# Performance work log

Hardware: AMD Instinct MI355X
Metric: run time of the kernel (lower is better)

## Reference

```python
import jax, jax.numpy as jnp
import numpy as np

B, L = 2, 4096
EMBED_DIM, NUM_HEADS, WINDOW = 1024, 16, 256
NUM_EXPERTS, TOP_K, FF_HIDDEN = 8, 2, 4096
ENTROPY_W, MAX_USAGE = 0.1, 0.3


def setup_inputs() -> dict:
    key = jax.random.key(0)
    ks = jax.random.split(key, 10)
    s = 0.02
    C, F, E = EMBED_DIM, FF_HIDDEN, NUM_EXPERTS
    return {
        "x": jax.random.normal(ks[0], (B, L, C), jnp.float32),
        "g1": jnp.ones((C,), jnp.float32), "b1": jnp.zeros((C,), jnp.float32),
        "g2": jnp.ones((C,), jnp.float32), "b2": jnp.zeros((C,), jnp.float32),
        "g3": jnp.ones((C,), jnp.float32), "b3": jnp.zeros((C,), jnp.float32),
        "Wqkv": jax.random.normal(ks[1], (C, 3 * C), jnp.float32) * s, "bqkv": jnp.zeros((3 * C,), jnp.float32),
        "Wo": jax.random.normal(ks[2], (C, C), jnp.float32) * s, "bo": jnp.zeros((C,), jnp.float32),
        "conv_w": jax.random.normal(ks[3], (C, C, 3), jnp.float32) * s, "conv_b": jnp.zeros((C,), jnp.float32),
        "gate_W": jax.random.normal(ks[4], (C, E), jnp.float32) * s, "gate_b": jnp.zeros((E,), jnp.float32),
        "expert_W": jax.random.normal(ks[5], (E, C, C), jnp.float32) * s, "expert_b": jnp.zeros((E, C), jnp.float32),
        "ff_W1": jax.random.normal(ks[6], (C, F), jnp.float32) * s, "ff_b1": jnp.zeros((F,), jnp.float32),
        "ff_W2": jax.random.normal(ks[7], (F, C), jnp.float32) * s, "ff_b2": jnp.zeros((C,), jnp.float32),
    }


def _ln(x, g, b):
    mu = x.mean(-1, keepdims=True)
    var = ((x - mu) ** 2).mean(-1, keepdims=True)
    return (x - mu) * jax.lax.rsqrt(var + 1e-5) * g + b


def _local_attn(x, Wqkv, bqkv, Wo, bo):
    # Faithful port of the unfold-based overlapping-window attention
    Bsz, Ln, C = x.shape
    hd = C // NUM_HEADS
    pad = (-Ln) % WINDOW
    xp = jnp.pad(x, ((0, 0), (0, pad), (0, 0)))
    Lp = Ln + pad
    qkv = (xp @ Wqkv + bqkv).reshape(Bsz, Lp, 3, NUM_HEADS, hd).transpose(2, 0, 3, 1, 4)
    q, k, v = qkv[0], qkv[1], qkv[2]  # [B,H,Lp,hd]
    step = WINDOW // 2  # bidirectional=True -> overlapping windows
    nw = (Lp - WINDOW) // step + 1
    idx = (jnp.arange(nw) * step)[:, None] + jnp.arange(WINDOW)[None, :]  # [nw,w]

    def win(t):
        # torch unfold(dim=2,size=w,step) puts window on LAST axis -> [B,H,nw,hd,w]
        return jnp.swapaxes(t[:, :, idx, :], -1, -2)

    qw, kw, vw = win(q), win(k), win(v)
    # q @ k^T over the window axis (exactly what the torch code computes)
    attn = jax.nn.softmax(jnp.einsum('bhnds,bhnes->bhnde', qw, kw) * hd ** -0.5, axis=-1)
    o = jnp.einsum('bhnde,bhnes->bhnds', attn, vw)  # [B,H,nw,hd,w]
    o = o.reshape(Bsz, NUM_HEADS, nw * WINDOW, hd).transpose(0, 2, 1, 3).reshape(Bsz, nw * WINDOW, C)
    return (o @ Wo + bo)[:, :Ln]


def _dconv(x, w, b):
    # Conv1d(C,C,k=3,dilation=2,padding='same'); w is [O,I,K]
    y = jax.lax.conv_general_dilated(jnp.swapaxes(x, 1, 2), w, (1,), 'SAME',
                                     rhs_dilation=(2,), dimension_numbers=('NCH', 'OIH', 'NCH'))
    return jnp.swapaxes(y + b[None, :, None], 1, 2)


def _moe(x, gW, gb, eW, eb):
    Bsz, S, C = x.shape
    N = Bsz * S
    xf = x.reshape(N, C)
    probs = jax.nn.softmax(xf @ gW + gb, axis=-1)
    entropy = -jnp.sum(probs * jnp.log(probs + 1e-10), axis=-1).mean()
    topk_p, topk_i = jax.lax.top_k(probs, TOP_K)  # [N,K]
    # dense-equivalent top-k dispatch: out[n] = sum_k p_k * expert_{i_k}(x_n)
    eo = jnp.einsum('nc,ech->neh', xf, eW) + eb  # [N,E,C]
    combine = jnp.zeros((N, NUM_EXPERTS), xf.dtype).at[jnp.arange(N)[:, None], topk_i].add(topk_p)
    out = jnp.einsum('neh,ne->nh', eo, combine)
    counts = jnp.zeros((NUM_EXPERTS,), jnp.float32).at[topk_i.reshape(-1)].add(1.0)
    penalty = jnp.sum(jax.nn.relu(counts / N - MAX_USAGE))
    return out.reshape(Bsz, S, C), ENTROPY_W * entropy + penalty


def reference(x, g1, b1, g2, b2, g3, b3, Wqkv, bqkv, Wo, bo, conv_w, conv_b,
              gate_W, gate_b, expert_W, expert_b, ff_W1, ff_b1, ff_W2, ff_b2):
    x = x + _local_attn(_ln(x, g1, b1), Wqkv, bqkv, Wo, bo)
    x = x + _dconv(_ln(x, g2, b2), conv_w, conv_b)
    moe_out, aux = _moe(_ln(x, g3, b3), gate_W, gate_b, expert_W, expert_b)
    x = x + moe_out
    x = x + (jax.nn.gelu(x @ ff_W1 + ff_b1, approximate=False) @ ff_W2 + ff_b2)
    return x, aux
```

## Files before the change

### kernel.cpp

```cpp
#include <hip/hip_runtime.h>
#include <cmath>

typedef _Float16 f16;
typedef __attribute__((ext_vector_type(8))) _Float16 f16x8;
typedef __attribute__((ext_vector_type(4))) _Float16 f16x4;
typedef __attribute__((ext_vector_type(4))) float f32x4;

struct TileInfo { int m0, mcnt, e, pad; };

__device__ __forceinline__ void gload16(const void* g, void* l) {
  __builtin_amdgcn_global_load_lds((const __attribute__((address_space(1))) void*)g,
                                   (__attribute__((address_space(3))) void*)l, 16, 0, 0);
}

__device__ __forceinline__ float fast_gelu(float u) {
  const float c = u * (0.7978845608028654f + 0.0356774081f * u * u);
  const float t = fminf(2.0f * c, 80.0f);
  const float e = __expf(t);
  return u * (e * __builtin_amdgcn_rcpf(e + 1.0f));
}

template<int NPASS, int MODE, int EPI>
__global__ __launch_bounds__(256)
void gemm_kernel(const f16* __restrict__ Ah, const f16* __restrict__ Al, int lda,
                 const f16* __restrict__ Bh, const f16* __restrict__ Bl, int ldb,
                 const float* __restrict__ bias, const float* __restrict__ res,
                 float* __restrict__ outf, f16* __restrict__ outh, int ldo, int K,
                 const int* __restrict__ rowmap, const TileInfo* __restrict__ table,
                 const char* __restrict__ zbuf) {
  __shared__ __align__(16) char lds[65536];

  const int tid  = threadIdx.x;
  const int wave = tid >> 6;
  const int lane = tid & 63;

  int m0, mcnt, eidx = 0;
  if (MODE == 2) {
    TileInfo ti = table[blockIdx.x];
    if (ti.mcnt <= 0) return;
    m0 = ti.m0; mcnt = ti.mcnt; eidx = ti.e;
  } else { m0 = blockIdx.x * 128; mcnt = 128; }
  const int n0 = blockIdx.y * 128;

  const f16* Bh_ = Bh;
  const float* bias_ = bias;
  size_t adelta = 0, bdelta = 0;
  if (NPASS == 3) {
    adelta = (size_t)((const char*)Al - (const char*)Ah);
    bdelta = (size_t)((const char*)Bl - (const char*)Bh);
  }
  if (MODE == 2) { Bh_ += ((size_t)eidx << 20); bias_ += eidx * 1024; }

  f32x4 acc[4][4] = {};
  const int wm  = (wave >> 1) * 64;
  const int wn  = (wave & 1) * 64;
  const int fr  = lane & 15;
  const int kgb = (lane >> 4) * 16;
  const int wuni = wave * 1024;

  const int sr    = tid / 8;
  const int cbyte = (tid % 8) * 16;

  if constexpr (NPASS == 1) {
    const char* aSrc[4];
    const char* bSrc[4];
    #pragma unroll
    for (int r = 0; r < 4; ++r) {
      const int mr  = sr + r * 32;
      const int cbs = cbyte ^ ((mr & 7) << 4);
      int gi = m0 + ((mr < mcnt) ? mr : (mcnt - 1));
      if (MODE == 1 || MODE == 2) gi = rowmap[gi];
      aSrc[r] = (const char*)Ah + (size_t)gi * lda * 2 + cbs;
      bSrc[r] = (const char*)Bh_ + (size_t)(n0 + mr) * ldb * 2 + cbs;
    }
    const int NT = K / 64;
    #pragma unroll
    for (int r = 0; r < 4; ++r) {
      gload16(aSrc[r], lds + r * 4096 + wuni);
      gload16(bSrc[r], lds + 16384 + r * 4096 + wuni);
    }
    #pragma unroll
    for (int r = 0; r < 4; ++r) {
      gload16(aSrc[r] + 128, lds + 32768 + r * 4096 + wuni);
      gload16(bSrc[r] + 128, lds + 32768 + 16384 + r * 4096 + wuni);
    }
    asm volatile("s_waitcnt vmcnt(8)" ::: "memory");
    __builtin_amdgcn_s_barrier();

    for (int kt = 0; kt < NT; ++kt) {
      const int c = kt & 1;
      const char* LAp = lds + c * 32768;
      const char* LBp = LAp + 16384;
      f16x8 ah[2][4], bh[2][4];
      #pragma unroll
      for (int kk = 0; kk < 2; ++kk) {
        #pragma unroll
        for (int i = 0; i < 4; ++i) {
          const int ar = wm + i * 16 + fr;
          ah[kk][i] = *(const f16x8*)(LAp + ar * 128 + ((kk * 64 + kgb) ^ ((ar & 7) << 4)));
          const int br = wn + i * 16 + fr;
          bh[kk][i] = *(const f16x8*)(LBp + br * 128 + ((kk * 64 + kgb) ^ ((br & 7) << 4)));
        }
      }
      asm volatile("s_waitcnt lgkmcnt(0)" ::: "memory");
      __builtin_amdgcn_s_barrier();
      if (kt + 2 < NT) {
        const size_t ko = (size_t)(kt + 2) * 128;
        #pragma unroll
        for (int r = 0; r < 4; ++r) {
          gload16(aSrc[r] + ko, lds + c * 32768 + r * 4096 + wuni);
          gload16(bSrc[r] + ko, lds + c * 32768 + 16384 + r * 4096 + wuni);
        }
      }
      #pragma unroll
      for (int kk = 0; kk < 2; ++kk)
        #pragma unroll
        for (int i = 0; i < 4; ++i)
          #pragma unroll
          for (int j = 0; j < 4; ++j)
            acc[i][j] = __builtin_amdgcn_mfma_f32_16x16x32_f16(ah[kk][i], bh[kk][j], acc[i][j], 0, 0, 0);
      if (kt + 2 < NT) asm volatile("s_waitcnt vmcnt(8)" ::: "memory");
      else             asm volatile("s_waitcnt vmcnt(0)" ::: "memory");
      __builtin_amdgcn_s_barrier();
    }
  } else {
    const char* aSrcB[4]; const char* bSrcB[4];
    int aRowC[4], aCbs[4];
    #pragma unroll
    for (int r = 0; r < 4; ++r) {
      const int mr  = sr + r * 32;
      const int cbs = cbyte ^ ((mr & 7) << 4);
      int gi = m0 + mr;
      if (MODE == 1) gi = rowmap[gi];
      if (MODE == 3) { aRowC[r] = gi; aCbs[r] = cbs; aSrcB[r] = nullptr; }
      else           { aSrcB[r] = (const char*)Ah + (size_t)gi * lda * 2 + cbs; aRowC[r] = 0; aCbs[r] = 0; }
      bSrcB[r] = (const char*)Bh_ + (size_t)(n0 + mr) * ldb * 2 + cbs;
    }
    const int NT = K / 64;
    f32x4 st[16];

    auto SLOAD = [&](int k0) {
      #pragma unroll
      for (int r = 0; r < 4; ++r) {
        const char* as; const char* asl;
        if (MODE == 3) {
          const int tap = k0 >> 10;
          const int kc  = k0 & 1023;
          const int tok = aRowC[r] & 4095;
          const int stk = tok + (tap - 1) * 2;
          if (stk >= 0 && stk < 4096) {
            as  = (const char*)Ah + (size_t)(aRowC[r] + (tap - 1) * 2) * 2048 + kc * 2 + aCbs[r];
            asl = as + adelta;
          } else { as = zbuf; asl = zbuf; }
        } else {
          as  = aSrcB[r] + (size_t)k0 * 2;
          asl = as + adelta;
        }
        st[r * 4 + 0] = *(const f32x4*)as;
        st[r * 4 + 1] = *(const f32x4*)asl;
        const char* bs = bSrcB[r] + (size_t)k0 * 2;
        st[r * 4 + 2] = *(const f32x4*)bs;
        st[r * 4 + 3] = *(const f32x4*)(bs + bdelta);
      }
    };
    auto SWRITE = [&]() {
      #pragma unroll
      for (int r = 0; r < 4; ++r) {
        *(f32x4*)(lds + 0     + r * 4096 + tid * 16) = st[r * 4 + 0];
        *(f32x4*)(lds + 16384 + r * 4096 + tid * 16) = st[r * 4 + 1];
        *(f32x4*)(lds + 32768 + r * 4096 + tid * 16) = st[r * 4 + 2];
        *(f32x4*)(lds + 49152 + r * 4096 + tid * 16) = st[r * 4 + 3];
      }
    };

    SLOAD(0);
    SWRITE();
    __syncthreads();

    for (int kt = 0; kt < NT; ++kt) {
      if (kt + 1 < NT) SLOAD((kt + 1) * 64);
      #pragma unroll
      for (int kk = 0; kk < 2; ++kk) {
        f16x8 ah[4], al[4], bh[4], bl[4];
        #pragma unroll
        for (int i = 0; i < 4; ++i) {
          const int ar = wm + i * 16 + fr;
          const int ao = ar * 128 + ((kk * 64 + kgb) ^ ((ar & 7) << 4));
          ah[i] = *(const f16x8*)(lds + ao);
          al[i] = *(const f16x8*)(lds + 16384 + ao);
          const int br = wn + i * 16 + fr;
          const int bo = br * 128 + ((kk * 64 + kgb) ^ ((br & 7) << 4));
          bh[i] = *(const f16x8*)(lds + 32768 + bo);
          bl[i] = *(const f16x8*)(lds + 49152 + bo);
        }
        #pragma unroll
        for (int i = 0; i < 4; ++i) {
          #pragma unroll
          for (int j = 0; j < 4; ++j) {
            acc[i][j] = __builtin_amdgcn_mfma_f32_16x16x32_f16(ah[i], bh[j], acc[i][j], 0, 0, 0);
            acc[i][j] = __builtin_amdgcn_mfma_f32_16x16x32_f16(ah[i], bl[j], acc[i][j], 0, 0, 0);
            acc[i][j] = __builtin_amdgcn_mfma_f32_16x16x32_f16(al[i], bh[j], acc[i][j], 0, 0, 0);
          }
        }
      }
      asm volatile("s_waitcnt lgkmcnt(0)" ::: "memory");
      __builtin_amdgcn_s_barrier();
      if (kt + 1 < NT) {
        SWRITE();
        asm volatile("s_waitcnt lgkmcnt(0)" ::: "memory");
      }
      __builtin_amdgcn_s_barrier();
    }
  }

  #pragma unroll
  for (int i = 0; i < 4; ++i) {
    const int mb = wm + i * 16 + (lane >> 4) * 4;
    #pragma unroll
    for (int j = 0; j < 4; ++j) {
      const int nc = n0 + wn + j * 16 + fr;
      const float bv = bias_[nc];
      #pragma unroll
      for (int q = 0; q < 4; ++q) {
        const int ml = mb + q;
        if (MODE == 2 && ml >= mcnt) continue;
        const size_t orow = (size_t)(m0 + ml);
        float v = acc[i][j][q] + bv;
        if (EPI == 1) v += res[orow * ldo + nc];
        if (EPI == 3) v = fast_gelu(v);
        if (EPI <= 1) outf[orow * ldo + nc] = v;
        else          outh[orow * ldo + nc] = (f16)v;
      }
    }
  }
}

template<int WLO, int WGATE>
__global__ __launch_bounds__(256)
void ln_kernel(const float* __restrict__ x, const float* __restrict__ g, const float* __restrict__ b,
               f16* __restrict__ oh, f16* __restrict__ ol,
               const float* __restrict__ gW, const float* __restrict__ gb,
               float* __restrict__ logits) {
  const int row = blockIdx.x;
  const int t = threadIdx.x;
  const float4 v = ((const float4*)(x + (size_t)row * 1024))[t];
  float s  = v.x + v.y + v.z + v.w;
  float ss = v.x * v.x + v.y * v.y + v.z * v.z + v.w * v.w;
  #pragma unroll
  for (int off = 32; off; off >>= 1) { s += __shfl_down(s, off, 64); ss += __shfl_down(ss, off, 64); }
  __shared__ float red[8];
  if ((t & 63) == 0) { red[t >> 6] = s; red[(t >> 6) + 4] = ss; }
  __syncthreads();
  s  = red[0] + red[1] + red[2] + red[3];
  ss = red[4] + red[5] + red[6] + red[7];
  const float mu  = s * (1.0f / 1024.0f);
  const float var = ss * (1.0f / 1024.0f) - mu * mu;
  const float inv = 1.0f / sqrtf(var + 1e-5f);
  const float4 gv = ((const float4*)g)[t];
  const float4 bv = ((const float4*)b)[t];
  float y[4];
  y[0] = (v.x - mu) * inv * gv.x + bv.x;
  y[1] = (v.y - mu) * inv * gv.y + bv.y;
  y[2] = (v.z - mu) * inv * gv.z + bv.z;
  y[3] = (v.w - mu) * inv * gv.w + bv.w;
  f16x4 hv;
  #pragma unroll
  for (int u = 0; u < 4; ++u) hv[u] = (f16)y[u];
  *(f16x4*)(oh + (size_t)row * 1024 + t * 4) = hv;
  if (WLO) {
    f16x4 lv;
    #pragma unroll
    for (int u = 0; u < 4; ++u) lv[u] = (f16)(y[u] - (float)hv[u]);
    *(f16x4*)(ol + (size_t)row * 1024 + t * 4) = lv;
  }
  if (WGATE) {
    const float* gr = gW + (size_t)(t * 4) * 8;
    float lg[8];
    #pragma unroll
    for (int e = 0; e < 8; ++e)
      lg[e] = y[0] * gr[e] + y[1] * gr[8 + e] + y[2] * gr[16 + e] + y[3] * gr[24 + e];
    #pragma unroll
    for (int m = 1; m < 64; m <<= 1)
      #pragma unroll
      for (int e = 0; e < 8; ++e) lg[e] += __shfl_xor(lg[e], m, 64);
    __shared__ float gred[4][8];
    if ((t & 63) == 0) {
      #pragma unroll
      for (int e = 0; e < 8; ++e) gred[t >> 6][e] = lg[e];
    }
    __syncthreads();
    if (t < 8)
      logits[(size_t)row * 8 + t] = gred[0][t] + gred[1][t] + gred[2][t] + gred[3][t] + gb[t];
  }
}

__global__ __launch_bounds__(512, 4)
void attn_kernel(const float* __restrict__ qkv, f16* __restrict__ oh, f16* __restrict__ ol) {
  __shared__ __align__(16) char sm[81920];
  const int bid = blockIdx.x;
  const int b = bid >> 8, h = (bid >> 4) & 15, n = bid & 15;
  const int t = threadIdx.x;
  const size_t rowbase = (size_t)(b * 2176 + n * 128);
  const char* qg = (const char*)(qkv + rowbase * 3072 + h * 64);
  const char* kg = qg + 4096;
  const char* vg = qg + 8192;

  const int srow = t >> 4;
  const int scol = (t & 15) * 16;
  const int wuni = (t >> 6) * 1024;

  const int dt = t >> 4;
  const int et = t & 15;
  float pacc[2][4] = {};

  for (int r = 0; r < 2; ++r) {
    #pragma unroll
    for (int p = 0; p < 4; ++p) {
      const size_t off = (size_t)(r * 128 + p * 32 + srow) * 12288 + scol;
      gload16(qg + off, sm + p * 8192 + wuni);
      gload16(kg + off, sm + 32768 + p * 8192 + wuni);
    }
    __syncthreads();
    #pragma unroll 4
    for (int s = 0; s < 128; ++s) {
      const float2 q2 = *(const float2*)(sm + s * 256 + dt * 8);
      const f32x4 k4 = *(const f32x4*)(sm + 32768 + s * 256 + et * 16);
      #pragma unroll
      for (int z = 0; z < 4; ++z) {
        pacc[0][z] += q2.x * k4[z];
        pacc[1][z] += q2.y * k4[z];
      }
    }
    __syncthreads();
  }

  #pragma unroll
  for (int i = 0; i < 2; ++i) {
    #pragma unroll
    for (int z = 0; z < 4; ++z) pacc[i][z] *= 0.125f;
    float m = fmaxf(fmaxf(pacc[i][0], pacc[i][1]), fmaxf(pacc[i][2], pacc[i][3]));
    m = fmaxf(m, __shfl_xor(m, 1, 16));
    m = fmaxf(m, __shfl_xor(m, 2, 16));
    m = fmaxf(m, __shfl_xor(m, 4, 16));
    m = fmaxf(m, __shfl_xor(m, 8, 16));
    float den = 0.0f;
    #pragma unroll
    for (int z = 0; z < 4; ++z) { pacc[i][z] = __expf(pacc[i][z] - m); den += pacc[i][z]; }
    den += __shfl_xor(den, 1, 16);
    den += __shfl_xor(den, 2, 16);
    den += __shfl_xor(den, 4, 16);
    den += __shfl_xor(den, 8, 16);
    const float dinv = 1.0f / den;
    f32x4 pv;
    #pragma unroll
    for (int z = 0; z < 4; ++z) pv[z] = pacc[i][z] * dinv;
    *(f32x4*)(sm + 65536 + (dt * 2 + i) * 256 + et * 16) = pv;
  }

  const int dt2 = t & 15;
  const int st  = t >> 4;
  const int ch  = h * 64 + (st & 15) * 4;
  const size_t rb2 = (size_t)(b * 4096 + n * 256);

  for (int c = 0; c < 2; ++c) {
    __syncthreads();
    #pragma unroll
    for (int p = 0; p < 4; ++p) {
      const size_t off = (size_t)(c * 128 + p * 32 + srow) * 12288 + scol;
      gload16(vg + off, sm + p * 8192 + wuni);
    }
    __syncthreads();
    float o[16];
    #pragma unroll
    for (int u = 0; u < 16; ++u) o[u] = 0.0f;
    #pragma unroll 2
    for (int e4 = 0; e4 < 16; ++e4) {
      f32x4 p4[4], v4[4];
      #pragma unroll
      for (int i = 0; i < 4; ++i)
        p4[i] = *(const f32x4*)(sm + 65536 + (dt2 * 4 + i) * 256 + e4 * 16);
      #pragma unroll
      for (int j = 0; j < 4; ++j)
        v4[j] = *(const f32x4*)(sm + (st * 4 + j) * 256 + e4 * 16);
      #pragma unroll
      for (int j = 0; j < 4; ++j)
        #pragma unroll
        for (int i = 0; i < 4; ++i) {
          o[j * 4 + i] += v4[j][0] * p4[i][0] + v4[j][1] * p4[i][1]
                        + v4[j][2] * p4[i][2] + v4[j][3] * p4[i][3];
        }
    }
    const int rq = c * 2 + (st >> 4);
    #pragma unroll
    for (int i = 0; i < 4; ++i) {
      const size_t row = rb2 + (size_t)(dt2 * 4 + i) * 4 + rq;
      f16x4 hv, lv;
      #pragma unroll
      for (int j = 0; j < 4; ++j) {
        const float val = o[j * 4 + i];
        hv[j] = (f16)val;
        lv[j] = (f16)(val - (float)hv[j]);
      }
      *(f16x4*)(oh + row * 1024 + ch) = hv;
      *(f16x4*)(ol + row * 1024 + ch) = lv;
    }
  }
}

template<int SPLIT>
__global__ __launch_bounds__(256)
void transpose_kernel(const float* __restrict__ in, int R, int Cc,
                      f16* __restrict__ oh, f16* __restrict__ ol) {
  __shared__ float tile[32][33];
  const size_t mat = (size_t)blockIdx.z * R * Cc;
  in += mat; oh += mat; if (SPLIT) ol += mat;
  const int tx = threadIdx.x & 31, ty = threadIdx.x >> 5;
  const int c = blockIdx.x * 32 + tx;
  #pragma unroll
  for (int j = 0; j < 32; j += 8) {
    const int r = blockIdx.y * 32 + ty + j;
    tile[ty + j][tx] = in[(size_t)r * Cc + c];
  }
  __syncthreads();
  const int rT = blockIdx.y * 32 + tx;
  #pragma unroll
  for (int j = 0; j < 32; j += 8) {
    const int cT = blockIdx.x * 32 + ty + j;
    const float v = tile[tx][ty + j];
    const f16 hv = (f16)v;
    oh[(size_t)cT * R + rT] = hv;
    if (SPLIT) ol[(size_t)cT * R + rT] = (f16)(v - (float)hv);
  }
}

__global__ __launch_bounds__(256)
void convw_kernel(const float* __restrict__ w, f16* __restrict__ oh, f16* __restrict__ ol) {
  const int id = blockIdx.x * 256 + threadIdx.x;
  const int o = id >> 10, i = id & 1023;
  const float* ws = w + (size_t)o * 3072 + i * 3;
  #pragma unroll
  for (int tap = 0; tap < 3; ++tap) {
    const float v = ws[tap];
    const f16 hv = (f16)v;
    const size_t oi = (size_t)o * 3072 + tap * 1024 + i;
    oh[oi] = hv;
    ol[oi] = (f16)(v - (float)hv);
  }
}

__global__ void qkvrows_kernel(int* __restrict__ rows) {
  const int r = blockIdx.x * 256 + threadIdx.x;
  if (r < 4352) rows[r] = (r >= 2176) ? (4096 + r - 2176) : r;
}

__global__ __launch_bounds__(256)
void gatefin_kernel(const float* __restrict__ logits, float* __restrict__ top2p,
                    int* __restrict__ top2i, float* __restrict__ ent,
                    int* __restrict__ counts) {
  __shared__ int hist[8];
  const int t = threadIdx.x;
  if (t < 8) hist[t] = 0;
  __syncthreads();
  const int token = blockIdx.x * 256 + t;
  float lg[8];
  const float4 l0 = ((const float4*)(logits + (size_t)token * 8))[0];
  const float4 l1 = ((const float4*)(logits + (size_t)token * 8))[1];
  lg[0] = l0.x; lg[1] = l0.y; lg[2] = l0.z; lg[3] = l0.w;
  lg[4] = l1.x; lg[5] = l1.y; lg[6] = l1.z; lg[7] = l1.w;
  int i0 = 0; float v0 = lg[0];
  #pragma unroll
  for (int e = 1; e < 8; ++e) if (lg[e] > v0) { v0 = lg[e]; i0 = e; }
  int i1 = 0; float v1 = -1e30f;
  #pragma unroll
  for (int e = 0; e < 8; ++e) if (e != i0 && lg[e] > v1) { v1 = lg[e]; i1 = e; }
  float den = 0.0f; float pr[8];
  #pragma unroll
  for (int e = 0; e < 8; ++e) { pr[e] = __expf(lg[e] - v0); den += pr[e]; }
  const float dinv = 1.0f / den;
  float H = 0.0f, p0 = 0.0f, p1 = 0.0f;
  #pragma unroll
  for (int e = 0; e < 8; ++e) {
    const float p = pr[e] * dinv;
    H -= p * __logf(p + 1e-10f);
    if (e == i0) p0 = p;
    if (e == i1) p1 = p;
  }
  ent[token] = H;
  top2p[token * 2] = p0; top2p[token * 2 + 1] = p1;
  top2i[token * 2] = i0; top2i[token * 2 + 1] = i1;
  atomicAdd(&hist[i0], 1);
  atomicAdd(&hist[i1], 1);
  __syncthreads();
  if (t < 8) atomicAdd(&counts[t], hist[t]);
}

__global__ __launch_bounds__(256)
void scan_kernel(const float* __restrict__ ent, const int* __restrict__ counts,
                 int* __restrict__ offs, TileInfo* __restrict__ table, float* __restrict__ auxout) {
  __shared__ float red[256];
  const int t = threadIdx.x;
  float s = 0.0f;
  for (int k = 0; k < 32; ++k) s += ent[t + (k << 8)];
  red[t] = s; __syncthreads();
  for (int hh = 128; hh > 0; hh >>= 1) { if (t < hh) red[t] += red[t + hh]; __syncthreads(); }
  if (t == 0) {
    const float entmean = red[0] * (1.0f / 8192.0f);
    float pen = 0.0f; int off = 0; int nt = 0;
    for (int e = 0; e < 8; ++e) {
      const int c = counts[e];
      offs[e] = off;
      for (int m = 0; m < c; m += 128) {
        table[nt].m0 = off + m;
        table[nt].mcnt = (c - m < 128) ? (c - m) : 128;
        table[nt].e = e; table[nt].pad = 0;
        ++nt;
      }
      off += c;
      const float fr = (float)c * (1.0f / 8192.0f) - 0.3f;
      pen += (fr > 0.0f) ? fr : 0.0f;
    }
    for (; nt < 160; ++nt) { table[nt].m0 = 0; table[nt].mcnt = 0; table[nt].e = 0; table[nt].pad = 0; }
    auxout[0] = 0.1f * entmean + pen;
  }
}

__global__ __launch_bounds__(256)
void scatter_kernel(const int* __restrict__ top2i, const int* __restrict__ offs,
                    int* __restrict__ fill, int* __restrict__ moe_rows,
                    int* __restrict__ row2slot) {
  __shared__ int hist[8];
  __shared__ int base[8];
  const int t = threadIdx.x;
  if (t < 8) hist[t] = 0;
  __syncthreads();
  const int id = blockIdx.x * 256 + t;
  const int e = top2i[id];
  const int myrank = atomicAdd(&hist[e], 1);
  __syncthreads();
  if (t < 8) base[t] = atomicAdd(&fill[t], hist[t]);
  __syncthreads();
  const int row = offs[e] + base[e] + myrank;
  moe_rows[row] = id >> 1;
  row2slot[id] = row;
}

__global__ __launch_bounds__(256)
void combine_kernel(const float* __restrict__ x2, const f16* __restrict__ eo,
                    const float* __restrict__ top2p, const int* __restrict__ row2slot,
                    float* __restrict__ x3, f16* __restrict__ x3h) {
  const int n = blockIdx.x;
  const int t = threadIdx.x;
  const int r0 = row2slot[n * 2], r1 = row2slot[n * 2 + 1];
  const float p0 = top2p[n * 2], p1 = top2p[n * 2 + 1];
  const float4 xv = ((const float4*)(x2 + (size_t)n * 1024))[t];
  const f16x4 e0 = ((const f16x4*)(eo + (size_t)r0 * 1024))[t];
  const f16x4 e1 = ((const f16x4*)(eo + (size_t)r1 * 1024))[t];
  float4 o;
  o.x = xv.x + p0 * (float)e0[0] + p1 * (float)e1[0];
  o.y = xv.y + p0 * (float)e0[1] + p1 * (float)e1[1];
  o.z = xv.z + p0 * (float)e0[2] + p1 * (float)e1[2];
  o.w = xv.w + p0 * (float)e0[3] + p1 * (float)e1[3];
  ((float4*)(x3 + (size_t)n * 1024))[t] = o;
  f16x4 hv; hv[0] = (f16)o.x; hv[1] = (f16)o.y; hv[2] = (f16)o.z; hv[3] = (f16)o.w;
  ((f16x4*)(x3h + (size_t)n * 1024))[t] = hv;
}

extern "C" void kernel_launch(void* const* d_in, const int* in_sizes, int n_in,
                              void* d_out, int out_size, void* d_ws, size_t ws_size,
                              hipStream_t stream) {
  (void)in_sizes; (void)n_in; (void)out_size; (void)ws_size;
  const float* x     = (const float*)d_in[0];
  const float* g1    = (const float*)d_in[1];
  const float* b1    = (const float*)d_in[2];
  const float* g2    = (const float*)d_in[3];
  const float* b2    = (const float*)d_in[4];
  const float* g3    = (const float*)d_in[5];
  const float* b3    = (const float*)d_in[6];
  const float* Wqkv  = (const float*)d_in[7];
  const float* bqkv  = (const float*)d_in[8];
  const float* Wo    = (const float*)d_in[9];
  const float* bo    = (const float*)d_in[10];
  const float* convw = (const float*)d_in[11];
  const float* convb = (const float*)d_in[12];
  const float* gateW = (const float*)d_in[13];
  const float* gateb = (const float*)d_in[14];
  const float* expW  = (const float*)d_in[15];
  const float* expb  = (const float*)d_in[16];
  const float* ffW1  = (const float*)d_in[17];
  const float* ffb1  = (const float*)d_in[18];
  const float* ffW2  = (const float*)d_in[19];
  const float* ffb2  = (const float*)d_in[20];
  float* out = (float*)d_out;

  char* W = (char*)d_ws;
  f16* wqkvT_h = (f16*)(W + 0);
  f16* wqkvT_l = (f16*)(W + 6291456);
  f16* woT_h   = (f16*)(W + 12582912);
  f16* woT_l   = (f16*)(W + 14680064);
  f16* wcvT_h  = (f16*)(W + 16777216);
  f16* wcvT_l  = (f16*)(W + 23068672);
  f16* wexpT   = (f16*)(W + 29360128);
  f16* wff1T   = (f16*)(W + 46137344);
  f16* wff2T   = (f16*)(W + 54525952);
  char* META   = W + 62914560;
  int* counts    = (int*)(META);
  int* fill      = (int*)(META + 32);
  int* offs      = (int*)(META + 64);
  TileInfo* table = (TileInfo*)(META + 128);
  char* zbuf     = META + 3072;
  int* qkv_rows  = (int*)(META + 4096);
  float* ent     = (float*)(META + 24576);
  float* top2p   = (float*)(META + 57344);
  int* top2i     = (int*)(META + 122880);
  int* moe_rows  = (int*)(META + 188416);
  int* row2slot  = (int*)(META + 253952);
  float* logits  = (float*)(META + 327680);
  char* SA = W + 63963136;
  char* SB = W + 97517568;
  char* SC = W + 164626432;
  char* SD = W + 198180864;
  char* SE = W + 231735296;

  f16* ln1h = (f16*)SA;            f16* ln1l = (f16*)(SA + 16777216);
  f16* ln2h = ln1h;                f16* ln2l = ln1l;
  f16* ln3h = ln1h;                f16* x3h  = (f16*)(SA + 16777216);
  float* qkvbuf = (float*)SB;
  float* x2buf  = (float*)SB;
  f16*   hbuf   = (f16*)SB;
  f16* attnh = (f16*)SC;           f16* attnl = (f16*)(SC + 16777216);
  float* x1 = (float*)SD;
  f16* eobuf = (f16*)SD;
  float* x3 = (float*)SE;

  hipMemsetAsync((void*)META, 0, 4096, stream);

  dim3 blk(256);
  transpose_kernel<1><<<dim3(96, 32, 1), blk, 0, stream>>>(Wqkv, 1024, 3072, wqkvT_h, wqkvT_l);
  transpose_kernel<1><<<dim3(32, 32, 1), blk, 0, stream>>>(Wo, 1024, 1024, woT_h, woT_l);
  convw_kernel<<<4096, blk, 0, stream>>>(convw, wcvT_h, wcvT_l);
  transpose_kernel<0><<<dim3(32, 32, 8), blk, 0, stream>>>(expW, 1024, 1024, wexpT, nullptr);
  transpose_kernel<0><<<dim3(128, 32, 1), blk, 0, stream>>>(ffW1, 1024, 4096, wff1T, nullptr);
  transpose_kernel<0><<<dim3(32, 128, 1), blk, 0, stream>>>(ffW2, 4096, 1024, wff2T, nullptr);
  qkvrows_kernel<<<17, blk, 0, stream>>>(qkv_rows);

  ln_kernel<1, 0><<<8192, blk, 0, stream>>>(x, g1, b1, ln1h, ln1l, nullptr, nullptr, nullptr);
  gemm_kernel<3, 1, 0><<<dim3(34, 24), blk, 0, stream>>>(ln1h, ln1l, 1024, wqkvT_h, wqkvT_l, 1024,
      bqkv, nullptr, qkvbuf, nullptr, 3072, 1024, qkv_rows, nullptr, nullptr);
  attn_kernel<<<512, dim3(512), 0, stream>>>(qkvbuf, attnh, attnl);
  gemm_kernel<3, 0, 1><<<dim3(64, 8), blk, 0, stream>>>(attnh, attnl, 1024, woT_h, woT_l, 1024,
      bo, x, x1, nullptr, 1024, 1024, nullptr, nullptr, nullptr);
  ln_kernel<1, 0><<<8192, blk, 0, stream>>>(x1, g2, b2, ln2h, ln2l, nullptr, nullptr, nullptr);
  gemm_kernel<3, 3, 1><<<dim3(64, 8), blk, 0, stream>>>(ln2h, ln2l, 1024, wcvT_h, wcvT_l, 3072,
      convb, x1, x2buf, nullptr, 1024, 3072, nullptr, nullptr, zbuf);
  ln_kernel<0, 1><<<8192, blk, 0, stream>>>(x2buf, g3, b3, ln3h, nullptr, gateW, gateb, logits);
  gatefin_kernel<<<32, blk, 0, stream>>>(logits, top2p, top2i, ent, counts);
  scan_kernel<<<1, blk, 0, stream>>>(ent, counts, offs, table, out + 8388608);
  scatter_kernel<<<64, blk, 0, stream>>>(top2i, offs, fill, moe_rows, row2slot);
  gemm_kernel<1, 2, 2><<<dim3(136, 8), blk, 0, stream>>>(ln3h, nullptr, 1024, wexpT, nullptr, 1024,
      expb, nullptr, nullptr, eobuf, 1024, 1024, moe_rows, table, nullptr);
  combine_kernel<<<8192, blk, 0, stream>>>(x2buf, eobuf, top2p, row2slot, x3, x3h);
  gemm_kernel<1, 0, 3><<<dim3(64, 32), blk, 0, stream>>>(x3h, nullptr, 1024, wff1T, nullptr, 1024,
      ffb1, nullptr, nullptr, hbuf, 4096, 1024, nullptr, nullptr, nullptr);
  gemm_kernel<1, 0, 1><<<dim3(64, 8), blk, 0, stream>>>(hbuf, nullptr, 4096, wff2T, nullptr, 4096,
      ffb2, x3, out, nullptr, 1024, 4096, nullptr, nullptr, nullptr);
}
```

Measured before the change: 765.3 us.

## Use direct global-to-LDS loads, swizzle block order, compact LN1 rows

The 3-pass GEMM path now loads tiles straight into LDS with global_load_lds instead of staging them through registers. Because there is only one LDS buffer, each step waits at a barrier before compute, which drops the register prefetch overlap. Block indices are remapped so consecutive launched blocks are spread across eight groups of the tile grid, aiming for better cache locality. LN1 now writes only the rows the QKV GEMM uses, in compacted order, which removes the rowmap kernel and halves LN1 work.

New measurement: 786.5 us. 2.8% more time.

```diff
diff --git a/kernel.cpp b/kernel.cpp
--- a/kernel.cpp
+++ b/kernel.cpp
@@ -34,13 +34,20 @@
   const int wave = tid >> 6;
   const int lane = tid & 63;
 
+  const int gx  = gridDim.x;
+  const int lid = blockIdx.x + blockIdx.y * gx;
+  const int per = (gx * gridDim.y) >> 3;
+  const int swz = (lid & 7) * per + (lid >> 3);
+  const int bx  = swz % gx;
+  const int by  = swz / gx;
+
   int m0, mcnt, eidx = 0;
   if (MODE == 2) {
-    TileInfo ti = table[blockIdx.x];
+    TileInfo ti = table[bx];
     if (ti.mcnt <= 0) return;
     m0 = ti.m0; mcnt = ti.mcnt; eidx = ti.e;
-  } else { m0 = blockIdx.x * 128; mcnt = 128; }
-  const int n0 = blockIdx.y * 128;
+  } else { m0 = bx * 128; mcnt = 128; }
+  const int n0 = by * 128;
 
   const f16* Bh_ = Bh;
   const float* bias_ = bias;
@@ -136,10 +143,7 @@
       else           { aSrcB[r] = (const char*)Ah + (size_t)gi * lda * 2 + cbs; aRowC[r] = 0; aCbs[r] = 0; }
       bSrcB[r] = (const char*)Bh_ + (size_t)(n0 + mr) * ldb * 2 + cbs;
     }
-    const int NT = K / 64;
-    f32x4 st[16];
-
-    auto SLOAD = [&](int k0) {
+    for (int k0 = 0; k0 < K; k0 += 64) {
       #pragma unroll
       for (int r = 0; r < 4; ++r) {
         const char* as; const char* asl;
@@ -156,29 +160,13 @@
           as  = aSrcB[r] + (size_t)k0 * 2;
           asl = as + adelta;
         }
-        st[r * 4 + 0] = *(const f32x4*)as;
-        st[r * 4 + 1] = *(const f32x4*)asl;
+        gload16(as,  lds + 0     + r * 4096 + wuni);
+        gload16(asl, lds + 16384 + r * 4096 + wuni);
         const char* bs = bSrcB[r] + (size_t)k0 * 2;
-        st[r * 4 + 2] = *(const f32x4*)bs;
-        st[r * 4 + 3] = *(const f32x4*)(bs + bdelta);
-      }
-    };
-    auto SWRITE = [&]() {
-      #pragma unroll
-      for (int r = 0; r < 4; ++r) {
-        *(f32x4*)(lds + 0     + r * 4096 + tid * 16) = st[r * 4 + 0];
-        *(f32x4*)(lds + 16384 + r * 4096 + tid * 16) = st[r * 4 + 1];
-        *(f32x4*)(lds + 32768 + r * 4096 + tid * 16) = st[r * 4 + 2];
-        *(f32x4*)(lds + 49152 + r * 4096 + tid * 16) = st[r * 4 + 3];
-      }
-    };
-
-    SLOAD(0);
-    SWRITE();
-    __syncthreads();
-
-    for (int kt = 0; kt < NT; ++kt) {
-      if (kt + 1 < NT) SLOAD((kt + 1) * 64);
+        gload16(bs,          lds + 32768 + r * 4096 + wuni);
+        gload16(bs + bdelta, lds + 49152 + r * 4096 + wuni);
+      }
+      __syncthreads();
       #pragma unroll
       for (int kk = 0; kk < 2; ++kk) {
         f16x8 ah[4], al[4], bh[4], bl[4];
@@ -203,13 +191,7 @@
           }
         }
       }
-      asm volatile("s_waitcnt lgkmcnt(0)" ::: "memory");
-      __builtin_amdgcn_s_barrier();
-      if (kt + 1 < NT) {
-        SWRITE();
-        asm volatile("s_waitcnt lgkmcnt(0)" ::: "memory");
-      }
-      __builtin_amdgcn_s_barrier();
+      __syncthreads();
     }
   }
 
@@ -235,15 +217,16 @@
   }
 }
 
-template<int WLO, int WGATE>
+template<int WLO, int WGATE, int COMPACT>
 __global__ __launch_bounds__(256)
 void ln_kernel(const float* __restrict__ x, const float* __restrict__ g, const float* __restrict__ b,
                f16* __restrict__ oh, f16* __restrict__ ol,
                const float* __restrict__ gW, const float* __restrict__ gb,
                float* __restrict__ logits) {
   const int row = blockIdx.x;
+  const int srow = COMPACT ? ((row < 2176) ? row : row + 1920) : row;
   const int t = threadIdx.x;
-  const float4 v = ((const float4*)(x + (size_t)row * 1024))[t];
+  const float4 v = ((const float4*)(x + (size_t)srow * 1024))[t];
   float s  = v.x + v.y + v.z + v.w;
   float ss = v.x * v.x + v.y * v.y + v.z * v.z + v.w * v.w;
   #pragma unroll
@@ -446,11 +429,6 @@
     oh[oi] = hv;
     ol[oi] = (f16)(v - (float)hv);
   }
-}
-
-__global__ void qkvrows_kernel(int* __restrict__ rows) {
-  const int r = blockIdx.x * 256 + threadIdx.x;
-  if (r < 4352) rows[r] = (r >= 2176) ? (4096 + r - 2176) : r;
 }
 
 __global__ __launch_bounds__(256)
@@ -608,7 +586,6 @@
   int* offs      = (int*)(META + 64);
   TileInfo* table = (TileInfo*)(META + 128);
   char* zbuf     = META + 3072;
-  int* qkv_rows  = (int*)(META + 4096);
   float* ent     = (float*)(META + 24576);
   float* top2p   = (float*)(META + 57344);
   int* top2i     = (int*)(META + 122880);
@@ -641,18 +618,17 @@
   transpose_kernel<0><<<dim3(32, 32, 8), blk, 0, stream>>>(expW, 1024, 1024, wexpT, nullptr);
   transpose_kernel<0><<<dim3(128, 32, 1), blk, 0, stream>>>(ffW1, 1024, 4096, wff1T, nullptr);
   transpose_kernel<0><<<dim3(32, 128, 1), blk, 0, stream>>>(ffW2, 4096, 1024, wff2T, nullptr);
-  qkvrows_kernel<<<17, blk, 0, stream>>>(qkv_rows);
-
-  ln_kernel<1, 0><<<8192, blk, 0, stream>>>(x, g1, b1, ln1h, ln1l, nullptr, nullptr, nullptr);
-  gemm_kernel<3, 1, 0><<<dim3(34, 24), blk, 0, stream>>>(ln1h, ln1l, 1024, wqkvT_h, wqkvT_l, 1024,
-      bqkv, nullptr, qkvbuf, nullptr, 3072, 1024, qkv_rows, nullptr, nullptr);
+
+  ln_kernel<1, 0, 1><<<4352, blk, 0, stream>>>(x, g1, b1, ln1h, ln1l, nullptr, nullptr, nullptr);
+  gemm_kernel<3, 0, 0><<<dim3(34, 24), blk, 0, stream>>>(ln1h, ln1l, 1024, wqkvT_h, wqkvT_l, 1024,
+      bqkv, nullptr, qkvbuf, nullptr, 3072, 1024, nullptr, nullptr, nullptr);
   attn_kernel<<<512, dim3(512), 0, stream>>>(qkvbuf, attnh, attnl);
   gemm_kernel<3, 0, 1><<<dim3(64, 8), blk, 0, stream>>>(attnh, attnl, 1024, woT_h, woT_l, 1024,
       bo, x, x1, nullptr, 1024, 1024, nullptr, nullptr, nullptr);
-  ln_kernel<1, 0><<<8192, blk, 0, stream>>>(x1, g2, b2, ln2h, ln2l, nullptr, nullptr, nullptr);
+  ln_kernel<1, 0, 0><<<8192, blk, 0, stream>>>(x1, g2, b2, ln2h, ln2l, nullptr, nullptr, nullptr);
   gemm_kernel<3, 3, 1><<<dim3(64, 8), blk, 0, stream>>>(ln2h, ln2l, 1024, wcvT_h, wcvT_l, 3072,
       convb, x1, x2buf, nullptr, 1024, 3072, nullptr, nullptr, zbuf);
-  ln_kernel<0, 1><<<8192, blk, 0, stream>>>(x2buf, g3, b3, ln3h, nullptr, gateW, gateb, logits);
+  ln_kernel<0, 1, 0><<<8192, blk, 0, stream>>>(x2buf, g3, b3, ln3h, nullptr, gateW, gateb, logits);
   gatefin_kernel<<<32, blk, 0, stream>>>(logits, top2p, top2i, ent, counts);
   scan_kernel<<<1, blk, 0, stream>>>(ent, counts, offs, table, out + 8388608);
   scatter_kernel<<<64, blk, 0, stream>>>(top2i, offs, fill, moe_rows, row2slot);
```
